# Kernel optimization log

Measured on AMD Instinct MI355X. Metric: run time of the kernel, lower is better.

## Reference

```python
import jax, jax.numpy as jnp
import numpy as np

V, H = 32000, 1024  # vocab / hidden, must match init_kwargs


def setup_inputs() -> dict:
    key = jax.random.key(0)
    ks = jax.random.split(key, 10)
    L, B, S = 32, 64, 16
    s = 1.0 / np.sqrt(H)
    emb_w = jax.random.normal(ks[0], (V, H), jnp.float32)
    emb_w = emb_w.at[0].set(0.0)  # padding_idx=0 row is zero
    return {
        "target_tensor": jax.random.randint(ks[1], (L, B), 0, V),
        "encoder_outputs": jax.random.normal(ks[2], (S, B, H), jnp.float32),
        "hidden": jax.random.normal(ks[3], (1, B, H), jnp.float32),
        "emb_w": emb_w,
        "w_ih": jax.random.uniform(ks[4], (3 * H, H), jnp.float32, -s, s),
        "w_hh": jax.random.uniform(ks[5], (3 * H, H), jnp.float32, -s, s),
        "b_ih": jax.random.uniform(ks[6], (3 * H,), jnp.float32, -s, s),
        "b_hh": jax.random.uniform(ks[7], (3 * H,), jnp.float32, -s, s),
        "fc_w": jax.random.uniform(ks[8], (V, H), jnp.float32, -s, s),
        "fc_b": jax.random.uniform(ks[9], (V,), jnp.float32, -s, s),
    }


def _gru_cell(x, h, w_ih, w_hh, b_ih, b_hh):
    # PyTorch GRU cell. x, h: [B, H]
    gi = x @ w_ih.T + b_ih            # [B, 3H]
    gh = h @ w_hh.T + b_hh            # [B, 3H]
    i_r, i_z, i_n = jnp.split(gi, 3, axis=-1)
    h_r, h_z, h_n = jnp.split(gh, 3, axis=-1)
    r = jax.nn.sigmoid(i_r + h_r)
    z = jax.nn.sigmoid(i_z + h_z)
    n = jnp.tanh(i_n + r * h_n)
    return (1.0 - z) * n + z * h


def reference(target_tensor, encoder_outputs, hidden, emb_w, w_ih, w_hh, b_ih, b_hh, fc_w, fc_b):
    L, B = target_tensor.shape
    # teacher forcing: step 0 uses all-ones token, step i uses target[i-1]
    ones0 = jnp.ones((1, B), dtype=target_tensor.dtype)
    inputs = jnp.concatenate([ones0, target_tensor[:-1]], axis=0)  # [L, B]
    h0 = hidden[0]  # [B, H]

    def step(h, idx):
        x = jax.nn.relu(emb_w[idx])            # [B, H] (dropout in eval mode)
        h_new = _gru_cell(x, h, w_ih, w_hh, b_ih, b_hh)
        return h_new, h_new

    h_last, outs = jax.lax.scan(step, h0, inputs)  # outs: [L, B, H]
    logits = jnp.einsum("lbh,vh->lbv", outs, fc_w) + fc_b  # [L, B, V]
    log_probs = jax.nn.log_softmax(logits, axis=-1)
    return log_probs, h_last[None]  # hidden: [1, B, H]
```

## Files before the change

### kernel.cpp

```cpp
#include <hip/hip_runtime.h>

typedef float  f32x4 __attribute__((ext_vector_type(4)));
typedef short  s16x8 __attribute__((ext_vector_type(8)));

#define AS1 __attribute__((address_space(1)))
#define AS3 __attribute__((address_space(3)))

__device__ __forceinline__ void gload_lds16(const void* g, void* l) {
  __builtin_amdgcn_global_load_lds((AS1 void*)(g), (AS3 void*)(l), 16, 0, 0);
}

__device__ __forceinline__ void mfma_bf16(f32x4& d, s16x8 a, s16x8 b) {
  asm volatile("v_mfma_f32_16x16x32_bf16 %0, %1, %2, %0" : "+v"(d) : "v"(a), "v"(b));
}

__device__ __forceinline__ void gload_b128(s16x8& d, const void* p) {
  asm volatile("global_load_dwordx4 %0, %1, off" : "=v"(d) : "v"(p));
}
__device__ __forceinline__ void gload_f128(f32x4& d, const void* p) {
  asm volatile("global_load_dwordx4 %0, %1, off" : "=v"(d) : "v"(p));
}

__device__ __forceinline__ unsigned short f2bf(float f) {
  union { float f; unsigned u; } v; v.f = f;
  unsigned u = v.u;
  unsigned r = u + 0x7fffu + ((u >> 16) & 1u);
  return (unsigned short)(r >> 16);
}
__device__ __forceinline__ float bf2f(unsigned short u) {
  union { unsigned u; float f; } v; v.u = ((unsigned)u) << 16; return v.f;
}

__launch_bounds__(256)
__global__ void cvt_bf16(const float* __restrict__ in, unsigned short* __restrict__ out, int n4) {
  for (int i = blockIdx.x * blockDim.x + threadIdx.x; i < n4; i += gridDim.x * blockDim.x) {
    float4 v = ((const float4*)in)[i];
    ushort4 u;
    u.x = f2bf(v.x); u.y = f2bf(v.y); u.z = f2bf(v.z); u.w = f2bf(v.w);
    ((ushort4*)out)[i] = u;
  }
}

__launch_bounds__(256)
__global__ void init_h(const float* __restrict__ hid, float* __restrict__ hA,
                       unsigned short* __restrict__ hbf) {
  int i = blockIdx.x * 256 + threadIdx.x;
  float4 v = ((const float4*)hid)[i];
  ((float4*)hA)[i] = v;
  ushort4 u; u.x = f2bf(v.x); u.y = f2bf(v.y); u.z = f2bf(v.z); u.w = f2bf(v.w);
  ((ushort4*)hbf)[i] = u;
}

__launch_bounds__(256)
__global__ void embed_relu(const int* __restrict__ tgt, const float* __restrict__ emb,
                           unsigned short* __restrict__ xbf) {
  int bid = blockIdx.x;
  int t = bid >> 6, b = bid & 63;
  int tok = (t == 0) ? 1 : tgt[(t - 1) * 64 + b];
  int c = threadIdx.x;
  float4 v = ((const float4*)(emb + (size_t)tok * 1024))[c];
  v.x = fmaxf(v.x, 0.f); v.y = fmaxf(v.y, 0.f); v.z = fmaxf(v.z, 0.f); v.w = fmaxf(v.w, 0.f);
  ushort4 u; u.x = f2bf(v.x); u.y = f2bf(v.y); u.z = f2bf(v.z); u.w = f2bf(v.w);
  ((ushort4*)(xbf + (size_t)bid * 1024))[c] = u;
}

template<bool STATS, bool OUTBF>
__launch_bounds__(256)
__global__ void gemm_bt(const unsigned short* __restrict__ A,
                        const unsigned short* __restrict__ B,
                        const float* __restrict__ bias,
                        float* __restrict__ Cf,
                        unsigned short* __restrict__ Cb,
                        float2* __restrict__ stats,
                        int N, int K, int mTiles, int nTilesTotal) {
  __shared__ unsigned short As[128 * 64];
  __shared__ unsigned short Bs[128 * 64];
  __shared__ float2 sstat[2][128];

  const int tid = threadIdx.x;
  int bid = blockIdx.x;
  {
    int q = gridDim.x >> 3;
    bid = (bid & 7) * q + (bid >> 3);
  }
  const int tileN = bid / mTiles;
  const int tileM = bid % mTiles;
  const int m0 = tileM * 128, n0 = tileN * 128;
  const int lane = tid & 63;
  const int w = tid >> 6, wr = w >> 1, wc = w & 1;
  const int lr = lane & 15, lg = lane >> 4;

  f32x4 acc[4][4];
#pragma unroll
  for (int m = 0; m < 4; ++m)
#pragma unroll
    for (int n = 0; n < 4; ++n) acc[m][n] = (f32x4){0.f, 0.f, 0.f, 0.f};

  const int crow = tid >> 3;
  const int cj   = tid & 7;

  for (int kt = 0; kt < K; kt += 64) {
#pragma unroll
    for (int it = 0; it < 4; ++it) {
      int row = it * 32 + crow;
      int sb = ((cj * 16) ^ ((row & 7) << 4)) >> 1;
      gload_lds16(A + (size_t)(m0 + row) * K + kt + sb, &As[row * 64 + cj * 8]);
      gload_lds16(B + (size_t)(n0 + row) * K + kt + sb, &Bs[row * 64 + cj * 8]);
    }
    __syncthreads();
#pragma unroll
    for (int kk = 0; kk < 2; ++kk) {
      s16x8 af[4], bfr[4];
#pragma unroll
      for (int m = 0; m < 4; ++m) {
        int row = wr * 64 + m * 16 + lr;
        int off = ((kk * 64 + lg * 16) ^ ((row & 7) << 4)) >> 1;
        af[m] = *reinterpret_cast<const s16x8*>(&As[row * 64 + off]);
      }
#pragma unroll
      for (int n = 0; n < 4; ++n) {
        int row = wc * 64 + n * 16 + lr;
        int off = ((kk * 64 + lg * 16) ^ ((row & 7) << 4)) >> 1;
        bfr[n] = *reinterpret_cast<const s16x8*>(&Bs[row * 64 + off]);
      }
#pragma unroll
      for (int m = 0; m < 4; ++m)
#pragma unroll
        for (int n = 0; n < 4; ++n) mfma_bf16(acc[m][n], af[m], bfr[n]);
    }
    __syncthreads();
  }

  float bv[4];
#pragma unroll
  for (int n = 0; n < 4; ++n) bv[n] = bias[n0 + wc * 64 + n * 16 + lr];
#pragma unroll
  for (int m = 0; m < 4; ++m)
#pragma unroll
    for (int n = 0; n < 4; ++n)
#pragma unroll
      for (int j = 0; j < 4; ++j) acc[m][n][j] += bv[n];

#pragma unroll
  for (int m = 0; m < 4; ++m) {
    int rbase = m0 + wr * 64 + m * 16 + lg * 4;
#pragma unroll
    for (int j = 0; j < 4; ++j) {
      size_t roff = (size_t)(rbase + j) * N;
#pragma unroll
      for (int n = 0; n < 4; ++n) {
        size_t idx = roff + n0 + wc * 64 + n * 16 + lr;
        if (OUTBF) Cb[idx] = f2bf(acc[m][n][j]);
        else       Cf[idx] = acc[m][n][j];
      }
    }
  }

  if (STATS) {
#pragma unroll
    for (int m = 0; m < 4; ++m) {
#pragma unroll
      for (int j = 0; j < 4; ++j) {
        float vmax = acc[m][0][j];
#pragma unroll
        for (int n = 1; n < 4; ++n) vmax = fmaxf(vmax, acc[m][n][j]);
#pragma unroll
        for (int s = 1; s < 16; s <<= 1) vmax = fmaxf(vmax, __shfl_xor(vmax, s, 64));
        float ss = 0.f;
#pragma unroll
        for (int n = 0; n < 4; ++n) ss += __expf(acc[m][n][j] - vmax);
#pragma unroll
        for (int s = 1; s < 16; s <<= 1) ss += __shfl_xor(ss, s, 64);
        if (lr == 0) sstat[wc][wr * 64 + m * 16 + lg * 4 + j] = make_float2(vmax, ss);
      }
    }
    __syncthreads();
    if (tid < 128) {
      float2 a = sstat[0][tid], b = sstat[1][tid];
      float Mx = fmaxf(a.x, b.x);
      float S = a.y * __expf(a.x - Mx) + b.y * __expf(b.x - Mx);
      stats[(size_t)(m0 + tid) * nTilesTotal + tileN] = make_float2(Mx, S);
    }
  }
}

__launch_bounds__(256, 1)
__global__ void gru_scan(const unsigned short* __restrict__ whh,
                         const float* __restrict__ gi,
                         const float* __restrict__ bhh,
                         float* __restrict__ h,
                         unsigned short* __restrict__ outs_bf,
                         unsigned* __restrict__ bar) {
  __shared__ char lds[96 * 1024];
  const int tid = threadIdx.x, lane = tid & 63, w = tid >> 6;
  const int lr = lane & 15, lg = lane >> 4;
  const int j0 = blockIdx.x * 16;

  for (int c = tid; c < 6144; c += 256) {
    int chunk = c >> 6, u = c & 63;
    int g = chunk >> 5, K = chunk & 31;
    gload_lds16(whh + (size_t)(g * 1024 + j0 + (u & 15)) * 1024 + K * 32 + (u >> 4) * 8,
                lds + (size_t)c * 16);
  }

  const int b  = w * 16 + lr;
  const int c0 = j0 + lg * 4;

  float4 bhr = *(const float4*)(bhh + c0);
  float4 bhz = *(const float4*)(bhh + 1024 + c0);
  float4 bhn = *(const float4*)(bhh + 2048 + c0);

  float4 hv = *(const float4*)(h + (size_t)b * 1024 + c0);
  f32x4 cr, cz, cn;
  {
    const float* g0 = gi + (size_t)b * 3072 + c0;
    cr = *(const f32x4*)(g0);
    cz = *(const f32x4*)(g0 + 1024);
    cn = *(const f32x4*)(g0 + 2048);
  }

  __syncthreads();

#define WAITV(n)                                               \
  asm volatile("s_waitcnt vmcnt(" #n ")" ::: "memory");        \
  __builtin_amdgcn_sched_barrier(0);
#define ISSUE8(q, ibase)                                       \
  _Pragma("unroll")                                            \
  for (int j = 0; j < 8; ++j)                                  \
    gload_b128(q[j], rowp + ((ibase) + j) * 4 + lg);
#define MFMA8(q, ibase)                                        \
  _Pragma("unroll")                                            \
  for (int j = 0; j < 8; ++j) {                                \
    _Pragma("unroll")                                          \
    for (int g = 0; g < 3; ++g) {                              \
      s16x8 wf = *reinterpret_cast<const s16x8*>(              \
          lds + (size_t)(g * 32 + (ibase) + j) * 1024 + lane * 16); \
      mfma_bf16(acc[g], wf, q[j]);                             \
    }                                                          \
  }

  for (int t = 0; t < 32; ++t) {
    const s16x8* rowp = (const s16x8*)(outs_bf + (size_t)t * 65536 + (size_t)b * 1024);

    f32x4 nr, nz, nn;
    {
      int tn = (t < 31) ? t + 1 : 31;
      const float* gn = gi + ((size_t)tn * 64 + b) * 3072 + c0;
      gload_f128(nr, gn);
      gload_f128(nz, gn + 1024);
      gload_f128(nn, gn + 2048);
    }
    s16x8 qa[8], qb[8];
    ISSUE8(qa, 0)
    ISSUE8(qb, 8)

    f32x4 acc[3];
#pragma unroll
    for (int g = 0; g < 3; ++g) acc[g] = (f32x4){0.f, 0.f, 0.f, 0.f};

    WAITV(8)
    MFMA8(qa, 0)
    ISSUE8(qa, 16)
    WAITV(8)
    MFMA8(qb, 8)
    ISSUE8(qb, 24)
    WAITV(8)
    MFMA8(qa, 16)
    WAITV(0)
    MFMA8(qb, 24)

    float hvv[4] = {hv.x, hv.y, hv.z, hv.w};
    float crr[4] = {cr[0], cr[1], cr[2], cr[3]}, czz[4] = {cz[0], cz[1], cz[2], cz[3]},
          cnn[4] = {cn[0], cn[1], cn[2], cn[3]};
    float brr[4] = {bhr.x, bhr.y, bhr.z, bhr.w}, bzz[4] = {bhz.x, bhz.y, bhz.z, bhz.w},
          bnn[4] = {bhn.x, bhn.y, bhn.z, bhn.w};
    unsigned long long pk = 0;
#pragma unroll
    for (int j = 0; j < 4; ++j) {
      float r = 1.f / (1.f + __expf(-(crr[j] + acc[0][j] + brr[j])));
      float z = 1.f / (1.f + __expf(-(czz[j] + acc[1][j] + bzz[j])));
      float n = tanhf(cnn[j] + r * (acc[2][j] + bnn[j]));
      hvv[j] = n + z * (hvv[j] - n);
      pk |= (unsigned long long)f2bf(hvv[j]) << (16 * j);
    }
    hv = (float4){hvv[0], hvv[1], hvv[2], hvv[3]};
    cr = nr; cz = nz; cn = nn;

    __hip_atomic_store(
        (unsigned long long*)(outs_bf + (size_t)(t + 1) * 65536 + (size_t)b * 1024 + c0),
        pk, __ATOMIC_RELAXED, __HIP_MEMORY_SCOPE_AGENT);

    if (t < 31) {
      asm volatile("s_waitcnt vmcnt(0)" ::: "memory");
      __syncthreads();
      if (tid == 0)
        __hip_atomic_store(&bar[blockIdx.x * 32], (unsigned)(t + 1),
                           __ATOMIC_RELAXED, __HIP_MEMORY_SCOPE_AGENT);
      if (tid < 64) {
        while (__hip_atomic_load(&bar[tid * 32], __ATOMIC_RELAXED,
                                 __HIP_MEMORY_SCOPE_AGENT) < (unsigned)(t + 1))
          __builtin_amdgcn_s_sleep(1);
      }
      __syncthreads();
    }
  }
#undef WAITV
#undef ISSUE8
#undef MFMA8

  *(float4*)(h + (size_t)b * 1024 + c0) = hv;
}

__launch_bounds__(256)
__global__ void reduce_logz(const float2* __restrict__ stats, float* __restrict__ logZ, int nt) {
  int gid = blockIdx.x * blockDim.x + threadIdx.x;
  int row = gid >> 6, lane = gid & 63;
  const float2* s = stats + (size_t)row * nt;
  float M = -3.4e38f;
  for (int i = lane; i < nt; i += 64) M = fmaxf(M, s[i].x);
#pragma unroll
  for (int sh = 1; sh < 64; sh <<= 1) M = fmaxf(M, __shfl_xor(M, sh, 64));
  float S = 0.f;
  for (int i = lane; i < nt; i += 64) S += s[i].y * __expf(s[i].x - M);
#pragma unroll
  for (int sh = 1; sh < 64; sh <<= 1) S += __shfl_xor(S, sh, 64);
  if (lane == 0) logZ[row] = M + logf(S);
}

__launch_bounds__(256)
__global__ void fixup_bf(const unsigned short* __restrict__ lbf, const float* __restrict__ logZ,
                         float* __restrict__ out) {
  const int n8 = 2048 * 32000 / 8;
  for (int i = blockIdx.x * 256 + threadIdx.x; i < n8; i += gridDim.x * 256) {
    s16x8 v = reinterpret_cast<const s16x8*>(lbf)[i];
    float z = logZ[i / 4000];
    float4 o0, o1;
    o0.x = bf2f((unsigned short)v[0]) - z; o0.y = bf2f((unsigned short)v[1]) - z;
    o0.z = bf2f((unsigned short)v[2]) - z; o0.w = bf2f((unsigned short)v[3]) - z;
    o1.x = bf2f((unsigned short)v[4]) - z; o1.y = bf2f((unsigned short)v[5]) - z;
    o1.z = bf2f((unsigned short)v[6]) - z; o1.w = bf2f((unsigned short)v[7]) - z;
    reinterpret_cast<float4*>(out)[2 * i]     = o0;
    reinterpret_cast<float4*>(out)[2 * i + 1] = o1;
  }
}

__launch_bounds__(256)
__global__ void fixup_rmw(float* __restrict__ out, const float* __restrict__ logZ) {
  const size_t total4 = 65536000u / 4u;
  for (size_t i = blockIdx.x * (size_t)blockDim.x + threadIdx.x; i < total4;
       i += (size_t)gridDim.x * blockDim.x) {
    float4 v = ((float4*)out)[i];
    int row = (int)((i * 4) / 32000);
    float z = logZ[row];
    v.x -= z; v.y -= z; v.z -= z; v.w -= z;
    ((float4*)out)[i] = v;
  }
}

__launch_bounds__(256)
__global__ void copy_h(const float* __restrict__ src, float* __restrict__ dst) {
  int i = blockIdx.x * 256 + threadIdx.x;
  ((float4*)dst)[i] = ((const float4*)src)[i];
}

extern "C" void kernel_launch(void* const* d_in, const int* in_sizes, int n_in,
                              void* d_out, int out_size, void* d_ws, size_t ws_size,
                              hipStream_t stream) {
  const int*   target = (const int*)d_in[0];
  const float* hidden = (const float*)d_in[2];
  const float* emb    = (const float*)d_in[3];
  const float* wih    = (const float*)d_in[4];
  const float* whh    = (const float*)d_in[5];
  const float* bih    = (const float*)d_in[6];
  const float* bhh    = (const float*)d_in[7];
  const float* fcw    = (const float*)d_in[8];
  const float* fcb    = (const float*)d_in[9];
  float* out = (float*)d_out;

  const int L = 32, B = 64, H = 1024, V = 32000;
  const int LB = L * B;
  const int NT_LOGITS = V / 128;
  const int MT = LB / 128;

  char* ws = (char*)d_ws;
  size_t off = 0;
  auto alloc = [&](size_t bytes) -> void* {
    void* p = ws + off;
    off += (bytes + 255) & ~(size_t)255;
    return p;
  };
  unsigned short* wih_bf  = (unsigned short*)alloc((size_t)3 * H * H * 2);
  unsigned short* whh_bf  = (unsigned short*)alloc((size_t)3 * H * H * 2);
  unsigned short* fcw_bf  = (unsigned short*)alloc((size_t)V * H * 2);
  unsigned short* x_bf    = (unsigned short*)alloc((size_t)LB * H * 2);
  unsigned short* outs_bf = (unsigned short*)alloc((size_t)(L + 1) * B * H * 2);
  float*          gi      = (float*)alloc((size_t)LB * 3 * H * 4);
  float*          hA      = (float*)alloc((size_t)B * H * 4);
  float2*         stats   = (float2*)alloc((size_t)LB * NT_LOGITS * 8);
  float*          logZ    = (float*)alloc((size_t)LB * 4);
  unsigned*       bar     = (unsigned*)alloc(64 * 128);
  size_t lbf_bytes = (size_t)LB * V * 2;
  unsigned short* lbf = (unsigned short*)(ws + off);
  bool big = (off + lbf_bytes) <= ws_size;
  (void)in_sizes; (void)n_in; (void)out_size;

  cvt_bf16<<<2048, 256, 0, stream>>>(wih, wih_bf, 3 * H * H / 4);
  cvt_bf16<<<2048, 256, 0, stream>>>(whh, whh_bf, 3 * H * H / 4);
  cvt_bf16<<<2048, 256, 0, stream>>>(fcw, fcw_bf, V * H / 4);

  init_h<<<64, 256, 0, stream>>>(hidden, hA, outs_bf);

  embed_relu<<<LB, 256, 0, stream>>>(target, emb, x_bf);

  gemm_bt<false, false><<<(3 * H / 128) * MT, 256, 0, stream>>>(
      x_bf, wih_bf, bih, gi, nullptr, nullptr, 3 * H, H, MT, 3 * H / 128);

  hipMemsetAsync(bar, 0, 64 * 128, stream);
  gru_scan<<<64, 256, 0, stream>>>(whh_bf, gi, bhh, hA, outs_bf, bar);

  if (big) {
    gemm_bt<true, true><<<NT_LOGITS * MT, 256, 0, stream>>>(
        outs_bf + (size_t)B * H, fcw_bf, fcb, nullptr, lbf, stats, V, H, MT, NT_LOGITS);
    reduce_logz<<<LB * 64 / 256, 256, 0, stream>>>(stats, logZ, NT_LOGITS);
    fixup_bf<<<2048, 256, 0, stream>>>(lbf, logZ, out);
  } else {
    gemm_bt<true, false><<<NT_LOGITS * MT, 256, 0, stream>>>(
        outs_bf + (size_t)B * H, fcw_bf, fcb, out, nullptr, stats, V, H, MT, NT_LOGITS);
    reduce_logz<<<LB * 64 / 256, 256, 0, stream>>>(stats, logZ, NT_LOGITS);
    fixup_rmw<<<2048, 256, 0, stream>>>(out, logZ);
  }

  copy_h<<<64, 256, 0, stream>>>(hA, out + (size_t)LB * V);
}
```

Baseline: 576.1 us.

## Fuse GRU scan with logits GEMM to overlap via progress flags

The GRU scan and the output-projection GEMM now run in one persistent launch of 240 blocks. The first 64 blocks run the recurrent scan and publish per-step progress flags. The remaining 176 blocks compute 128x128 logits tiles, each waiting until the time steps it needs have been produced. This overlaps the latency-bound sequential scan with the bandwidth-heavy logits GEMM, where before they ran back to back. The risks are deadlock if not all 240 blocks are co-resident, and the GEMM blocks contending with the scan for memory bandwidth and slowing the critical path.

```diff
diff --git a/kernel.cpp b/kernel.cpp
--- a/kernel.cpp
+++ b/kernel.cpp
@@ -184,42 +184,52 @@
   }
 }
 
+template<bool OUTBF>
 __launch_bounds__(256, 1)
-__global__ void gru_scan(const unsigned short* __restrict__ whh,
-                         const float* __restrict__ gi,
-                         const float* __restrict__ bhh,
-                         float* __restrict__ h,
-                         unsigned short* __restrict__ outs_bf,
-                         unsigned* __restrict__ bar) {
-  __shared__ char lds[96 * 1024];
+__global__ void scan_fused(const unsigned short* __restrict__ whh,
+                           const float* __restrict__ gi,
+                           const float* __restrict__ bhh,
+                           float* __restrict__ h,
+                           unsigned short* __restrict__ outs_bf,
+                           unsigned* __restrict__ bar,
+                           const unsigned short* __restrict__ fcw,
+                           const float* __restrict__ fcb,
+                           float* __restrict__ Cf,
+                           unsigned short* __restrict__ Cb,
+                           float2* __restrict__ stats) {
+  __shared__ char smem[96 * 1024];
   const int tid = threadIdx.x, lane = tid & 63, w = tid >> 6;
   const int lr = lane & 15, lg = lane >> 4;
-  const int j0 = blockIdx.x * 16;
-
-  for (int c = tid; c < 6144; c += 256) {
-    int chunk = c >> 6, u = c & 63;
-    int g = chunk >> 5, K = chunk & 31;
-    gload_lds16(whh + (size_t)(g * 1024 + j0 + (u & 15)) * 1024 + K * 32 + (u >> 4) * 8,
-                lds + (size_t)c * 16);
-  }
-
-  const int b  = w * 16 + lr;
-  const int c0 = j0 + lg * 4;
-
-  float4 bhr = *(const float4*)(bhh + c0);
-  float4 bhz = *(const float4*)(bhh + 1024 + c0);
-  float4 bhn = *(const float4*)(bhh + 2048 + c0);
-
-  float4 hv = *(const float4*)(h + (size_t)b * 1024 + c0);
-  f32x4 cr, cz, cn;
-  {
-    const float* g0 = gi + (size_t)b * 3072 + c0;
-    cr = *(const f32x4*)(g0);
-    cz = *(const f32x4*)(g0 + 1024);
-    cn = *(const f32x4*)(g0 + 2048);
-  }
-
-  __syncthreads();
+  const int bid = blockIdx.x;
+
+  if (bid < 64) {
+    char* lds = smem;
+    const int j0 = bid * 16;
+
+    for (int c = tid; c < 6144; c += 256) {
+      int chunk = c >> 6, u = c & 63;
+      int g = chunk >> 5, K = chunk & 31;
+      gload_lds16(whh + (size_t)(g * 1024 + j0 + (u & 15)) * 1024 + K * 32 + (u >> 4) * 8,
+                  lds + (size_t)c * 16);
+    }
+
+    const int b  = w * 16 + lr;
+    const int c0 = j0 + lg * 4;
+
+    float4 bhr = *(const float4*)(bhh + c0);
+    float4 bhz = *(const float4*)(bhh + 1024 + c0);
+    float4 bhn = *(const float4*)(bhh + 2048 + c0);
+
+    float4 hv = *(const float4*)(h + (size_t)b * 1024 + c0);
+    f32x4 cr, cz, cn;
+    {
+      const float* g0 = gi + (size_t)b * 3072 + c0;
+      cr = *(const f32x4*)(g0);
+      cz = *(const f32x4*)(g0 + 1024);
+      cn = *(const f32x4*)(g0 + 2048);
+    }
+
+    __syncthreads();
 
 #define WAITV(n)                                               \
   asm volatile("s_waitcnt vmcnt(" #n ")" ::: "memory");        \
@@ -239,76 +249,203 @@
     }                                                          \
   }
 
-  for (int t = 0; t < 32; ++t) {
-    const s16x8* rowp = (const s16x8*)(outs_bf + (size_t)t * 65536 + (size_t)b * 1024);
-
-    f32x4 nr, nz, nn;
-    {
-      int tn = (t < 31) ? t + 1 : 31;
-      const float* gn = gi + ((size_t)tn * 64 + b) * 3072 + c0;
-      gload_f128(nr, gn);
-      gload_f128(nz, gn + 1024);
-      gload_f128(nn, gn + 2048);
-    }
-    s16x8 qa[8], qb[8];
-    ISSUE8(qa, 0)
-    ISSUE8(qb, 8)
-
-    f32x4 acc[3];
-#pragma unroll
-    for (int g = 0; g < 3; ++g) acc[g] = (f32x4){0.f, 0.f, 0.f, 0.f};
-
-    WAITV(8)
-    MFMA8(qa, 0)
-    ISSUE8(qa, 16)
-    WAITV(8)
-    MFMA8(qb, 8)
-    ISSUE8(qb, 24)
-    WAITV(8)
-    MFMA8(qa, 16)
-    WAITV(0)
-    MFMA8(qb, 24)
-
-    float hvv[4] = {hv.x, hv.y, hv.z, hv.w};
-    float crr[4] = {cr[0], cr[1], cr[2], cr[3]}, czz[4] = {cz[0], cz[1], cz[2], cz[3]},
-          cnn[4] = {cn[0], cn[1], cn[2], cn[3]};
-    float brr[4] = {bhr.x, bhr.y, bhr.z, bhr.w}, bzz[4] = {bhz.x, bhz.y, bhz.z, bhz.w},
-          bnn[4] = {bhn.x, bhn.y, bhn.z, bhn.w};
-    unsigned long long pk = 0;
-#pragma unroll
-    for (int j = 0; j < 4; ++j) {
-      float r = 1.f / (1.f + __expf(-(crr[j] + acc[0][j] + brr[j])));
-      float z = 1.f / (1.f + __expf(-(czz[j] + acc[1][j] + bzz[j])));
-      float n = tanhf(cnn[j] + r * (acc[2][j] + bnn[j]));
-      hvv[j] = n + z * (hvv[j] - n);
-      pk |= (unsigned long long)f2bf(hvv[j]) << (16 * j);
-    }
-    hv = (float4){hvv[0], hvv[1], hvv[2], hvv[3]};
-    cr = nr; cz = nz; cn = nn;
-
-    __hip_atomic_store(
-        (unsigned long long*)(outs_bf + (size_t)(t + 1) * 65536 + (size_t)b * 1024 + c0),
-        pk, __ATOMIC_RELAXED, __HIP_MEMORY_SCOPE_AGENT);
-
-    if (t < 31) {
+    for (int t = 0; t < 32; ++t) {
+      const s16x8* rowp = (const s16x8*)(outs_bf + (size_t)t * 65536 + (size_t)b * 1024);
+
+      f32x4 nr, nz, nn;
+      {
+        int tn = (t < 31) ? t + 1 : 31;
+        const float* gn = gi + ((size_t)tn * 64 + b) * 3072 + c0;
+        gload_f128(nr, gn);
+        gload_f128(nz, gn + 1024);
+        gload_f128(nn, gn + 2048);
+      }
+      s16x8 qa[8], qb[8];
+      ISSUE8(qa, 0)
+      ISSUE8(qb, 8)
+
+      f32x4 acc[3];
+#pragma unroll
+      for (int g = 0; g < 3; ++g) acc[g] = (f32x4){0.f, 0.f, 0.f, 0.f};
+
+      WAITV(8)
+      MFMA8(qa, 0)
+      ISSUE8(qa, 16)
+      WAITV(8)
+      MFMA8(qb, 8)
+      ISSUE8(qb, 24)
+      WAITV(8)
+      MFMA8(qa, 16)
+      WAITV(0)
+      MFMA8(qb, 24)
+
+      float hvv[4] = {hv.x, hv.y, hv.z, hv.w};
+      float crr[4] = {cr[0], cr[1], cr[2], cr[3]}, czz[4] = {cz[0], cz[1], cz[2], cz[3]},
+            cnn[4] = {cn[0], cn[1], cn[2], cn[3]};
+      float brr[4] = {bhr.x, bhr.y, bhr.z, bhr.w}, bzz[4] = {bhz.x, bhz.y, bhz.z, bhz.w},
+            bnn[4] = {bhn.x, bhn.y, bhn.z, bhn.w};
+      unsigned long long pk = 0;
+#pragma unroll
+      for (int j = 0; j < 4; ++j) {
+        float r = 1.f / (1.f + __expf(-(crr[j] + acc[0][j] + brr[j])));
+        float z = 1.f / (1.f + __expf(-(czz[j] + acc[1][j] + bzz[j])));
+        float n = tanhf(cnn[j] + r * (acc[2][j] + bnn[j]));
+        hvv[j] = n + z * (hvv[j] - n);
+        pk |= (unsigned long long)f2bf(hvv[j]) << (16 * j);
+      }
+      hv = (float4){hvv[0], hvv[1], hvv[2], hvv[3]};
+      cr = nr; cz = nz; cn = nn;
+
+      __hip_atomic_store(
+          (unsigned long long*)(outs_bf + (size_t)(t + 1) * 65536 + (size_t)b * 1024 + c0),
+          pk, __ATOMIC_RELAXED, __HIP_MEMORY_SCOPE_AGENT);
+
       asm volatile("s_waitcnt vmcnt(0)" ::: "memory");
       __syncthreads();
       if (tid == 0)
-        __hip_atomic_store(&bar[blockIdx.x * 32], (unsigned)(t + 1),
+        __hip_atomic_store(&bar[bid * 32], (unsigned)(t + 1),
                            __ATOMIC_RELAXED, __HIP_MEMORY_SCOPE_AGENT);
-      if (tid < 64) {
-        while (__hip_atomic_load(&bar[tid * 32], __ATOMIC_RELAXED,
-                                 __HIP_MEMORY_SCOPE_AGENT) < (unsigned)(t + 1))
-          __builtin_amdgcn_s_sleep(1);
-      }
-      __syncthreads();
-    }
-  }
+      if (t < 31) {
+        if (tid < 64) {
+          while (__hip_atomic_load(&bar[tid * 32], __ATOMIC_RELAXED,
+                                   __HIP_MEMORY_SCOPE_AGENT) < (unsigned)(t + 1))
+            __builtin_amdgcn_s_sleep(1);
+        }
+        __syncthreads();
+      }
+    }
 #undef WAITV
 #undef ISSUE8
 #undef MFMA8
 
-  *(float4*)(h + (size_t)b * 1024 + c0) = hv;
+    *(float4*)(h + (size_t)b * 1024 + c0) = hv;
+
+  } else {
+    unsigned short* As0 = (unsigned short*)smem;
+    unsigned short* Bs0 = (unsigned short*)(smem + 16384);
+    unsigned short* As1 = (unsigned short*)(smem + 32768);
+    unsigned short* Bs1 = (unsigned short*)(smem + 49152);
+    float2* sstat = (float2*)(smem + 65536);
+
+    const unsigned short* Ag = outs_bf + 65536;
+    const unsigned short* Bg = fcw;
+    const int cb = bid - 64;
+    const int wr = w >> 1, wc = w & 1;
+    const int crow = tid >> 3, cj = tid & 7;
+
+#define CSTAGE(Asp, Bsp, kt)                                                        \
+    _Pragma("unroll")                                                               \
+    for (int it = 0; it < 4; ++it) {                                                \
+      int row = it * 32 + crow;                                                     \
+      int sb = ((cj * 16) ^ ((row & 7) << 4)) >> 1;                                 \
+      gload_lds16(Ag + (size_t)(m0 + row) * 1024 + (kt) + sb, Asp + row * 64 + cj * 8); \
+      gload_lds16(Bg + (size_t)(n0 + row) * 1024 + (kt) + sb, Bsp + row * 64 + cj * 8); \
+    }
+#define CCOMP(Asp, Bsp)                                                             \
+    _Pragma("unroll")                                                               \
+    for (int kk = 0; kk < 2; ++kk) {                                                \
+      s16x8 af[4], bfr[4];                                                          \
+      _Pragma("unroll")                                                             \
+      for (int m = 0; m < 4; ++m) {                                                 \
+        int row = wr * 64 + m * 16 + lr;                                            \
+        int off = ((kk * 64 + lg * 16) ^ ((row & 7) << 4)) >> 1;                    \
+        af[m] = *reinterpret_cast<const s16x8*>(&Asp[row * 64 + off]);              \
+      }                                                                             \
+      _Pragma("unroll")                                                             \
+      for (int n = 0; n < 4; ++n) {                                                 \
+        int row = wc * 64 + n * 16 + lr;                                            \
+        int off = ((kk * 64 + lg * 16) ^ ((row & 7) << 4)) >> 1;                    \
+        bfr[n] = *reinterpret_cast<const s16x8*>(&Bsp[row * 64 + off]);             \
+      }                                                                             \
+      _Pragma("unroll")                                                             \
+      for (int m = 0; m < 4; ++m)                                                   \
+        _Pragma("unroll")                                                           \
+        for (int n = 0; n < 4; ++n) mfma_bf16(acc[m][n], af[m], bfr[n]);            \
+    }
+
+    for (int tau = cb; tau < 4000; tau += 176) {
+      int mt = tau / 250, nt = tau - mt * 250;
+      int m0 = mt * 128, n0 = nt * 128;
+
+      unsigned need = 2u * (unsigned)mt + 2u;
+      while (!__all(__hip_atomic_load(&bar[lane * 32], __ATOMIC_RELAXED,
+                                      __HIP_MEMORY_SCOPE_AGENT) >= need))
+        __builtin_amdgcn_s_sleep(2);
+
+      f32x4 acc[4][4];
+#pragma unroll
+      for (int m = 0; m < 4; ++m)
+#pragma unroll
+        for (int n = 0; n < 4; ++n) acc[m][n] = (f32x4){0.f, 0.f, 0.f, 0.f};
+
+      CSTAGE(As0, Bs0, 0)
+      __syncthreads();
+#pragma unroll 2
+      for (int ki = 0; ki < 16; ++ki) {
+        if (ki & 1) {
+          if (ki < 15) CSTAGE(As0, Bs0, (ki + 1) * 64)
+          CCOMP(As1, Bs1)
+        } else {
+          if (ki < 15) CSTAGE(As1, Bs1, (ki + 1) * 64)
+          CCOMP(As0, Bs0)
+        }
+        __syncthreads();
+      }
+
+      float bv[4];
+#pragma unroll
+      for (int n = 0; n < 4; ++n) bv[n] = fcb[n0 + wc * 64 + n * 16 + lr];
+#pragma unroll
+      for (int m = 0; m < 4; ++m)
+#pragma unroll
+        for (int n = 0; n < 4; ++n)
+#pragma unroll
+          for (int j = 0; j < 4; ++j) acc[m][n][j] += bv[n];
+
+#pragma unroll
+      for (int m = 0; m < 4; ++m) {
+        int rbase = m0 + wr * 64 + m * 16 + lg * 4;
+#pragma unroll
+        for (int j = 0; j < 4; ++j) {
+          size_t roff = (size_t)(rbase + j) * 32000;
+#pragma unroll
+          for (int n = 0; n < 4; ++n) {
+            size_t idx = roff + n0 + wc * 64 + n * 16 + lr;
+            if (OUTBF) Cb[idx] = f2bf(acc[m][n][j]);
+            else       Cf[idx] = acc[m][n][j];
+          }
+        }
+      }
+
+#pragma unroll
+      for (int m = 0; m < 4; ++m) {
+#pragma unroll
+        for (int j = 0; j < 4; ++j) {
+          float vmax = acc[m][0][j];
+#pragma unroll
+          for (int n = 1; n < 4; ++n) vmax = fmaxf(vmax, acc[m][n][j]);
+#pragma unroll
+          for (int s = 1; s < 16; s <<= 1) vmax = fmaxf(vmax, __shfl_xor(vmax, s, 64));
+          float ss = 0.f;
+#pragma unroll
+          for (int n = 0; n < 4; ++n) ss += __expf(acc[m][n][j] - vmax);
+#pragma unroll
+          for (int s = 1; s < 16; s <<= 1) ss += __shfl_xor(ss, s, 64);
+          if (lr == 0) sstat[wc * 128 + wr * 64 + m * 16 + lg * 4 + j] = make_float2(vmax, ss);
+        }
+      }
+      __syncthreads();
+      if (tid < 128) {
+        float2 a = sstat[tid], b2 = sstat[128 + tid];
+        float Mx = fmaxf(a.x, b2.x);
+        float S = a.y * __expf(a.x - Mx) + b2.y * __expf(b2.x - Mx);
+        stats[(size_t)(m0 + tid) * 250 + nt] = make_float2(Mx, S);
+      }
+      __syncthreads();
+    }
+#undef CSTAGE
+#undef CCOMP
+  }
 }
 
 __launch_bounds__(256)
@@ -416,16 +553,14 @@
       x_bf, wih_bf, bih, gi, nullptr, nullptr, 3 * H, H, MT, 3 * H / 128);
 
   hipMemsetAsync(bar, 0, 64 * 128, stream);
-  gru_scan<<<64, 256, 0, stream>>>(whh_bf, gi, bhh, hA, outs_bf, bar);
-
   if (big) {
-    gemm_bt<true, true><<<NT_LOGITS * MT, 256, 0, stream>>>(
-        outs_bf + (size_t)B * H, fcw_bf, fcb, nullptr, lbf, stats, V, H, MT, NT_LOGITS);
+    scan_fused<true><<<240, 256, 0, stream>>>(
+        whh_bf, gi, bhh, hA, outs_bf, bar, fcw_bf, fcb, nullptr, lbf, stats);
     reduce_logz<<<LB * 64 / 256, 256, 0, stream>>>(stats, logZ, NT_LOGITS);
     fixup_bf<<<2048, 256, 0, stream>>>(lbf, logZ, out);
   } else {
-    gemm_bt<true, false><<<NT_LOGITS * MT, 256, 0, stream>>>(
-        outs_bf + (size_t)B * H, fcw_bf, fcb, out, nullptr, stats, V, H, MT, NT_LOGITS);
+    scan_fused<false><<<240, 256, 0, stream>>>(
+        whh_bf, gi, bhh, hA, outs_bf, bar, fcw_bf, fcb, out, nullptr, stats);
     reduce_logz<<<LB * 64 / 256, 256, 0, stream>>>(stats, logZ, NT_LOGITS);
     fixup_rmw<<<2048, 256, 0, stream>>>(out, logZ);
   }
```

After: 581.7 us (median of 2 runs). Within noise of the previous version (+1.0%).

## Fuse GRU scan with logits GEMM so output projection overlaps recurrence

Applied to the files above, without the earlier changes.

Merges the sequential GRU scan and the vocab projection GEMM into one persistent kernel of 240 blocks. The first 64 blocks run the recurrence and publish per-step progress flags. The remaining 176 blocks compute 64x128 logit tiles per wave, spinning until the needed timestep rows are ready, and write partial softmax stats. This hides the logits GEMM behind the latency-bound scan, but the GEMM now uses only 176 blocks with per-wave tiles and its own pipelining, which may be slower than the original full-grid GEMM. Spin-polling may also contend with the scan's barrier.

```diff
diff --git a/kernel.cpp b/kernel.cpp
--- a/kernel.cpp
+++ b/kernel.cpp
@@ -30,6 +30,10 @@
 __device__ __forceinline__ float bf2f(unsigned short u) {
   union { unsigned u; float f; } v; v.u = ((unsigned)u) << 16; return v.f;
 }
+
+#define WAITV(n)                                               \
+  asm volatile("s_waitcnt vmcnt(" #n ")" ::: "memory");        \
+  __builtin_amdgcn_sched_barrier(0);
 
 __launch_bounds__(256)
 __global__ void cvt_bf16(const float* __restrict__ in, unsigned short* __restrict__ out, int n4) {
@@ -184,46 +188,53 @@
   }
 }
 
+template<bool OUTBF>
 __launch_bounds__(256, 1)
-__global__ void gru_scan(const unsigned short* __restrict__ whh,
-                         const float* __restrict__ gi,
-                         const float* __restrict__ bhh,
-                         float* __restrict__ h,
-                         unsigned short* __restrict__ outs_bf,
-                         unsigned* __restrict__ bar) {
-  __shared__ char lds[96 * 1024];
+__global__ void scan_fused(const unsigned short* __restrict__ whh,
+                           const float* __restrict__ gi,
+                           const float* __restrict__ bhh,
+                           float* __restrict__ h,
+                           unsigned short* __restrict__ outs_bf,
+                           unsigned* __restrict__ bar,
+                           const unsigned short* __restrict__ fcw,
+                           const float* __restrict__ fcb,
+                           float* __restrict__ Cf,
+                           unsigned short* __restrict__ Cb,
+                           float2* __restrict__ stats) {
+  __shared__ char smem[96 * 1024];
   const int tid = threadIdx.x, lane = tid & 63, w = tid >> 6;
   const int lr = lane & 15, lg = lane >> 4;
-  const int j0 = blockIdx.x * 16;
-
-  for (int c = tid; c < 6144; c += 256) {
-    int chunk = c >> 6, u = c & 63;
-    int g = chunk >> 5, K = chunk & 31;
-    gload_lds16(whh + (size_t)(g * 1024 + j0 + (u & 15)) * 1024 + K * 32 + (u >> 4) * 8,
-                lds + (size_t)c * 16);
-  }
-
-  const int b  = w * 16 + lr;
-  const int c0 = j0 + lg * 4;
-
-  float4 bhr = *(const float4*)(bhh + c0);
-  float4 bhz = *(const float4*)(bhh + 1024 + c0);
-  float4 bhn = *(const float4*)(bhh + 2048 + c0);
-
-  float4 hv = *(const float4*)(h + (size_t)b * 1024 + c0);
-  f32x4 cr, cz, cn;
-  {
-    const float* g0 = gi + (size_t)b * 3072 + c0;
-    cr = *(const f32x4*)(g0);
-    cz = *(const f32x4*)(g0 + 1024);
-    cn = *(const f32x4*)(g0 + 2048);
-  }
-
-  __syncthreads();
-
-#define WAITV(n)                                               \
-  asm volatile("s_waitcnt vmcnt(" #n ")" ::: "memory");        \
-  __builtin_amdgcn_sched_barrier(0);
+  const int bid = blockIdx.x;
+
+  if (bid < 64) {
+    char* lds = smem;
+    const int j0 = bid * 16;
+
+    for (int c = tid; c < 6144; c += 256) {
+      int chunk = c >> 6, u = c & 63;
+      int g = chunk >> 5, K = chunk & 31;
+      gload_lds16(whh + (size_t)(g * 1024 + j0 + (u & 15)) * 1024 + K * 32 + (u >> 4) * 8,
+                  lds + (size_t)c * 16);
+    }
+
+    const int b  = w * 16 + lr;
+    const int c0 = j0 + lg * 4;
+
+    float4 bhr = *(const float4*)(bhh + c0);
+    float4 bhz = *(const float4*)(bhh + 1024 + c0);
+    float4 bhn = *(const float4*)(bhh + 2048 + c0);
+
+    float4 hv = *(const float4*)(h + (size_t)b * 1024 + c0);
+    f32x4 cr, cz, cn;
+    {
+      const float* g0 = gi + (size_t)b * 3072 + c0;
+      cr = *(const f32x4*)(g0);
+      cz = *(const f32x4*)(g0 + 1024);
+      cn = *(const f32x4*)(g0 + 2048);
+    }
+
+    __syncthreads();
+
 #define ISSUE8(q, ibase)                                       \
   _Pragma("unroll")                                            \
   for (int j = 0; j < 8; ++j)                                  \
@@ -239,76 +250,181 @@
     }                                                          \
   }
 
-  for (int t = 0; t < 32; ++t) {
-    const s16x8* rowp = (const s16x8*)(outs_bf + (size_t)t * 65536 + (size_t)b * 1024);
-
-    f32x4 nr, nz, nn;
-    {
-      int tn = (t < 31) ? t + 1 : 31;
-      const float* gn = gi + ((size_t)tn * 64 + b) * 3072 + c0;
-      gload_f128(nr, gn);
-      gload_f128(nz, gn + 1024);
-      gload_f128(nn, gn + 2048);
-    }
-    s16x8 qa[8], qb[8];
-    ISSUE8(qa, 0)
-    ISSUE8(qb, 8)
-
-    f32x4 acc[3];
-#pragma unroll
-    for (int g = 0; g < 3; ++g) acc[g] = (f32x4){0.f, 0.f, 0.f, 0.f};
-
-    WAITV(8)
-    MFMA8(qa, 0)
-    ISSUE8(qa, 16)
-    WAITV(8)
-    MFMA8(qb, 8)
-    ISSUE8(qb, 24)
-    WAITV(8)
-    MFMA8(qa, 16)
-    WAITV(0)
-    MFMA8(qb, 24)
-
-    float hvv[4] = {hv.x, hv.y, hv.z, hv.w};
-    float crr[4] = {cr[0], cr[1], cr[2], cr[3]}, czz[4] = {cz[0], cz[1], cz[2], cz[3]},
-          cnn[4] = {cn[0], cn[1], cn[2], cn[3]};
-    float brr[4] = {bhr.x, bhr.y, bhr.z, bhr.w}, bzz[4] = {bhz.x, bhz.y, bhz.z, bhz.w},
-          bnn[4] = {bhn.x, bhn.y, bhn.z, bhn.w};
-    unsigned long long pk = 0;
-#pragma unroll
-    for (int j = 0; j < 4; ++j) {
-      float r = 1.f / (1.f + __expf(-(crr[j] + acc[0][j] + brr[j])));
-      float z = 1.f / (1.f + __expf(-(czz[j] + acc[1][j] + bzz[j])));
-      float n = tanhf(cnn[j] + r * (acc[2][j] + bnn[j]));
-      hvv[j] = n + z * (hvv[j] - n);
-      pk |= (unsigned long long)f2bf(hvv[j]) << (16 * j);
-    }
-    hv = (float4){hvv[0], hvv[1], hvv[2], hvv[3]};
-    cr = nr; cz = nz; cn = nn;
-
-    __hip_atomic_store(
-        (unsigned long long*)(outs_bf + (size_t)(t + 1) * 65536 + (size_t)b * 1024 + c0),
-        pk, __ATOMIC_RELAXED, __HIP_MEMORY_SCOPE_AGENT);
-
-    if (t < 31) {
+    for (int t = 0; t < 32; ++t) {
+      const s16x8* rowp = (const s16x8*)(outs_bf + (size_t)t * 65536 + (size_t)b * 1024);
+
+      f32x4 nr, nz, nn;
+      {
+        int tn = (t < 31) ? t + 1 : 31;
+        const float* gn = gi + ((size_t)tn * 64 + b) * 3072 + c0;
+        gload_f128(nr, gn);
+        gload_f128(nz, gn + 1024);
+        gload_f128(nn, gn + 2048);
+      }
+      s16x8 qa[8], qb[8];
+      ISSUE8(qa, 0)
+      ISSUE8(qb, 8)
+
+      f32x4 acc[3];
+#pragma unroll
+      for (int g = 0; g < 3; ++g) acc[g] = (f32x4){0.f, 0.f, 0.f, 0.f};
+
+      WAITV(8)
+      MFMA8(qa, 0)
+      ISSUE8(qa, 16)
+      WAITV(8)
+      MFMA8(qb, 8)
+      ISSUE8(qb, 24)
+      WAITV(8)
+      MFMA8(qa, 16)
+      WAITV(0)
+      MFMA8(qb, 24)
+
+      float hvv[4] = {hv.x, hv.y, hv.z, hv.w};
+      float crr[4] = {cr[0], cr[1], cr[2], cr[3]}, czz[4] = {cz[0], cz[1], cz[2], cz[3]},
+            cnn[4] = {cn[0], cn[1], cn[2], cn[3]};
+      float brr[4] = {bhr.x, bhr.y, bhr.z, bhr.w}, bzz[4] = {bhz.x, bhz.y, bhz.z, bhz.w},
+            bnn[4] = {bhn.x, bhn.y, bhn.z, bhn.w};
+      unsigned long long pk = 0;
+#pragma unroll
+      for (int j = 0; j < 4; ++j) {
+        float r = 1.f / (1.f + __expf(-(crr[j] + acc[0][j] + brr[j])));
+        float z = 1.f / (1.f + __expf(-(czz[j] + acc[1][j] + bzz[j])));
+        float n = tanhf(cnn[j] + r * (acc[2][j] + bnn[j]));
+        hvv[j] = n + z * (hvv[j] - n);
+        pk |= (unsigned long long)f2bf(hvv[j]) << (16 * j);
+      }
+      hv = (float4){hvv[0], hvv[1], hvv[2], hvv[3]};
+      cr = nr; cz = nz; cn = nn;
+
+      __hip_atomic_store(
+          (unsigned long long*)(outs_bf + (size_t)(t + 1) * 65536 + (size_t)b * 1024 + c0),
+          pk, __ATOMIC_RELAXED, __HIP_MEMORY_SCOPE_AGENT);
+
       asm volatile("s_waitcnt vmcnt(0)" ::: "memory");
       __syncthreads();
       if (tid == 0)
-        __hip_atomic_store(&bar[blockIdx.x * 32], (unsigned)(t + 1),
+        __hip_atomic_store(&bar[bid * 32], (unsigned)(t + 1),
                            __ATOMIC_RELAXED, __HIP_MEMORY_SCOPE_AGENT);
-      if (tid < 64) {
-        while (__hip_atomic_load(&bar[tid * 32], __ATOMIC_RELAXED,
-                                 __HIP_MEMORY_SCOPE_AGENT) < (unsigned)(t + 1))
-          __builtin_amdgcn_s_sleep(1);
-      }
-      __syncthreads();
-    }
-  }
-#undef WAITV
+      if (t < 31) {
+        if (tid < 64) {
+          while (__hip_atomic_load(&bar[tid * 32], __ATOMIC_RELAXED,
+                                   __HIP_MEMORY_SCOPE_AGENT) < (unsigned)(t + 1))
+            __builtin_amdgcn_s_sleep(1);
+        }
+        __syncthreads();
+      }
+    }
 #undef ISSUE8
 #undef MFMA8
 
-  *(float4*)(h + (size_t)b * 1024 + c0) = hv;
+    *(float4*)(h + (size_t)b * 1024 + c0) = hv;
+
+  } else {
+    const int wid = (bid - 64) * 4 + w;
+    char* Ab0 = smem + w * 24576;
+    char* Bb0 = Ab0 + 4096;
+    char* Ab1 = Ab0 + 12288;
+    char* Bb1 = Ab1 + 4096;
+    const int l4 = lane >> 2, sl = lane & 3;
+    const int ksw = (sl ^ ((l4 >> 1) & 3)) * 8;
+    const int xrd = (lg ^ ((lr >> 1) & 3)) * 16;
+    const unsigned short* Abase = outs_bf + 65536;
+
+#define CSTG(AB, BB, asrc, bsrc, kt)                                                    \
+    _Pragma("unroll")                                                                   \
+    for (int i = 0; i < 4; ++i)                                                         \
+      gload_lds16((asrc) + (size_t)(i * 16 + l4) * 1024 + (kt) + ksw,                   \
+                  (AB) + i * 1024 + lane * 16);                                         \
+    _Pragma("unroll")                                                                   \
+    for (int i = 0; i < 8; ++i)                                                         \
+      gload_lds16((bsrc) + (size_t)(i * 16 + l4) * 1024 + (kt) + ksw,                   \
+                  (BB) + i * 1024 + lane * 16);
+#define FRAGM(AB, BB)                                                                   \
+    { s16x8 af[4], bfr[8];                                                              \
+      _Pragma("unroll")                                                                 \
+      for (int m = 0; m < 4; ++m)                                                       \
+        af[m] = *reinterpret_cast<const s16x8*>((AB) + (m * 16 + lr) * 64 + xrd);       \
+      _Pragma("unroll")                                                                 \
+      for (int n = 0; n < 8; ++n)                                                       \
+        bfr[n] = *reinterpret_cast<const s16x8*>((BB) + (n * 16 + lr) * 64 + xrd);      \
+      _Pragma("unroll")                                                                 \
+      for (int m = 0; m < 4; ++m)                                                       \
+        _Pragma("unroll")                                                               \
+        for (int n = 0; n < 8; ++n) mfma_bf16(acc[m][n], af[m], bfr[n]); }
+
+    for (int tau = wid; tau < 8000; tau += 704) {
+      const int mt = tau / 250, nt = tau - mt * 250;
+      const int n0 = nt * 128;
+      const unsigned short* asrc = Abase + (size_t)(mt * 64) * 1024;
+      const unsigned short* bsrc = fcw + (size_t)n0 * 1024;
+
+      {
+        unsigned need = (unsigned)mt + 1u;
+        while (!__all(__hip_atomic_load(&bar[lane * 32], __ATOMIC_RELAXED,
+                                        __HIP_MEMORY_SCOPE_AGENT) >= need))
+          __builtin_amdgcn_s_sleep(8);
+      }
+
+      f32x4 acc[4][8];
+#pragma unroll
+      for (int m = 0; m < 4; ++m)
+#pragma unroll
+        for (int n = 0; n < 8; ++n) acc[m][n] = (f32x4){0.f, 0.f, 0.f, 0.f};
+
+      CSTG(Ab0, Bb0, asrc, bsrc, 0)
+      for (int k2 = 0; k2 < 16; ++k2) {
+        CSTG(Ab1, Bb1, asrc, bsrc, (2 * k2 + 1) * 32)
+        WAITV(12)
+        FRAGM(Ab0, Bb0)
+        if (k2 < 15) {
+          CSTG(Ab0, Bb0, asrc, bsrc, (2 * k2 + 2) * 32)
+          WAITV(12)
+        } else {
+          WAITV(0)
+        }
+        FRAGM(Ab1, Bb1)
+      }
+
+      float bv[8];
+#pragma unroll
+      for (int n = 0; n < 8; ++n) bv[n] = fcb[n0 + n * 16 + lr];
+#pragma unroll
+      for (int m = 0; m < 4; ++m)
+#pragma unroll
+        for (int n = 0; n < 8; ++n)
+#pragma unroll
+          for (int j = 0; j < 4; ++j) acc[m][n][j] += bv[n];
+
+#pragma unroll
+      for (int m = 0; m < 4; ++m) {
+#pragma unroll
+        for (int j = 0; j < 4; ++j) {
+          size_t row = (size_t)(mt * 64 + m * 16 + lg * 4 + j);
+          size_t roff = row * 32000;
+#pragma unroll
+          for (int n = 0; n < 8; ++n) {
+            size_t idx = roff + n0 + n * 16 + lr;
+            if (OUTBF) Cb[idx] = f2bf(acc[m][n][j]);
+            else       Cf[idx] = acc[m][n][j];
+          }
+          float vmax = acc[m][0][j];
+#pragma unroll
+          for (int n = 1; n < 8; ++n) vmax = fmaxf(vmax, acc[m][n][j]);
+#pragma unroll
+          for (int s = 1; s < 16; s <<= 1) vmax = fmaxf(vmax, __shfl_xor(vmax, s, 64));
+          float ss = 0.f;
+#pragma unroll
+          for (int n = 0; n < 8; ++n) ss += __expf(acc[m][n][j] - vmax);
+#pragma unroll
+          for (int s = 1; s < 16; s <<= 1) ss += __shfl_xor(ss, s, 64);
+          if (lr == 0) stats[row * 250 + nt] = make_float2(vmax, ss);
+        }
+      }
+    }
+#undef CSTG
+#undef FRAGM
+  }
 }
 
 __launch_bounds__(256)
@@ -416,16 +532,14 @@
       x_bf, wih_bf, bih, gi, nullptr, nullptr, 3 * H, H, MT, 3 * H / 128);
 
   hipMemsetAsync(bar, 0, 64 * 128, stream);
-  gru_scan<<<64, 256, 0, stream>>>(whh_bf, gi, bhh, hA, outs_bf, bar);
-
   if (big) {
-    gemm_bt<true, true><<<NT_LOGITS * MT, 256, 0, stream>>>(
-        outs_bf + (size_t)B * H, fcw_bf, fcb, nullptr, lbf, stats, V, H, MT, NT_LOGITS);
+    scan_fused<true><<<240, 256, 0, stream>>>(
+        whh_bf, gi, bhh, hA, outs_bf, bar, fcw_bf, fcb, nullptr, lbf, stats);
     reduce_logz<<<LB * 64 / 256, 256, 0, stream>>>(stats, logZ, NT_LOGITS);
     fixup_bf<<<2048, 256, 0, stream>>>(lbf, logZ, out);
   } else {
-    gemm_bt<true, false><<<NT_LOGITS * MT, 256, 0, stream>>>(
-        outs_bf + (size_t)B * H, fcw_bf, fcb, out, nullptr, stats, V, H, MT, NT_LOGITS);
+    scan_fused<false><<<240, 256, 0, stream>>>(
+        whh_bf, gi, bhh, hA, outs_bf, bar, fcw_bf, fcb, out, nullptr, stats);
     reduce_logz<<<LB * 64 / 256, 256, 0, stream>>>(stats, logZ, NT_LOGITS);
     fixup_rmw<<<2048, 256, 0, stream>>>(out, logZ);
   }
```

After: 601.5 us, median of 2. +4.4%, slower.
